# Kernel tuning notes

Measured on AMD Instinct MI355X. Metric: run time of the kernel, lower is better.

Reference implementation:

```python
import jax, jax.numpy as jnp
import numpy as np

N, D = 200000, 256          # num nodes, feature dim
B, NEG = 1024, 64           # batch size, neg_sample_size
S1, S2 = 25, 10             # num_samples for layer 0 and layer 1
OUT = 128                   # per-layer output_dim (concat -> 2*OUT emitted)


def setup_inputs() -> dict:
    key = jax.random.key(0)
    ks = jax.random.split(key, 14)
    inp = {
        "features": jax.random.normal(ks[0], (N, D), jnp.float32),
        "W_self0": jax.random.normal(ks[1], (D, OUT), jnp.float32) / np.sqrt(D).astype(np.float32),
        "W_neigh0": jax.random.normal(ks[2], (D, OUT), jnp.float32) / np.sqrt(D).astype(np.float32),
        "W_self1": jax.random.normal(ks[3], (2 * OUT, OUT), jnp.float32) / np.sqrt(2 * OUT).astype(np.float32),
        "W_neigh1": jax.random.normal(ks[4], (2 * OUT, OUT), jnp.float32) / np.sqrt(2 * OUT).astype(np.float32),
        "s1_0": jax.random.randint(ks[5], (B,), 0, N),
        "s1_1": jax.random.randint(ks[6], (B * S2,), 0, N),
        "s1_2": jax.random.randint(ks[7], (B * S2 * S1,), 0, N),
        "s2_0": jax.random.randint(ks[8], (B,), 0, N),
        "s2_1": jax.random.randint(ks[9], (B * S2,), 0, N),
        "s2_2": jax.random.randint(ks[10], (B * S2 * S1,), 0, N),
        "n_0": jax.random.randint(ks[11], (NEG,), 0, N),
        "n_1": jax.random.randint(ks[12], (NEG * S2,), 0, N),
        "n_2": jax.random.randint(ks[13], (NEG * S2 * S1,), 0, N),
    }
    return inp


def _agg(h_self, h_neigh, Ws, Wn, act):
    """GraphSAGE mean aggregator with concat=True: [M, 2*OUT]."""
    return act(jnp.concatenate([h_self @ Ws, jnp.mean(h_neigh, axis=1) @ Wn], axis=-1))


def _l2norm(x):
    return x / jnp.maximum(jnp.linalg.norm(x, axis=1, keepdims=True), 1e-12)


def reference(features, W_self0, W_neigh0, W_self1, W_neigh1,
              s1_0, s1_1, s1_2, s2_0, s2_1, s2_2, n_0, n_1, n_2):
    def encode(i0, i1, i2, bs):
        h0 = features[i0]                     # [bs, D]
        h1 = features[i1]                     # [bs*S2, D]
        h2 = features[i2]                     # [bs*S2*S1, D]
        # layer 0 (ReLU), applied at hop 0 and hop 1
        g0 = _agg(h0, h1.reshape(bs, S2, D), W_self0, W_neigh0, jax.nn.relu)          # [bs, 2*OUT]
        g1 = _agg(h1, h2.reshape(bs * S2, S1, D), W_self0, W_neigh0, jax.nn.relu)     # [bs*S2, 2*OUT]
        # layer 1 (identity act), hop 0 only
        out = _agg(g0, g1.reshape(bs, S2, 2 * OUT), W_self1, W_neigh1, lambda x: x)   # [bs, 2*OUT]
        return _l2norm(out)

    u1 = encode(s1_0, s1_1, s1_2, B)
    u2 = encode(s2_0, s2_1, s2_2, B)
    un = encode(n_0, n_1, n_2, NEG)

    aff = jnp.sum(u1 * u2, axis=-1)          # [B] positive affinities
    neg_aff = u1 @ un.T                      # [B, NEG]
    # sigmoid cross-entropy: pos label 1, neg label 0
    loss = (jnp.sum(jax.nn.softplus(-aff)) + jnp.sum(jax.nn.softplus(neg_aff))) / B
    return loss, aff, neg_aff, u1
```

## Files before the change

kernel.cpp:

```cpp
#include <hip/hip_runtime.h>
#include <math.h>

#define DD   256
#define BB   1024
#define NEGN 64
#define S1N  25
#define S2N  10
#define OUTN 128
#define NB   (2 * BB + NEGN)
#define NREF1 (2 * BB * S2N + NEGN * S2N)
#define NREF  (NREF1 + NB)
#define NREFP 23280

typedef unsigned int  uint;
typedef unsigned short ushort;
typedef short bf16x8 __attribute__((ext_vector_type(8)));
typedef float f32x4  __attribute__((ext_vector_type(4)));

__device__ __forceinline__ ushort f2bf(float x) {
    uint u = __float_as_uint(x);
    u += 0x7FFFu + ((u >> 16) & 1u);
    return (ushort)(u >> 16);
}
__device__ __forceinline__ float bflo(uint v) { return __uint_as_float(v << 16); }
__device__ __forceinline__ float bfhi(uint v) { return __uint_as_float(v & 0xFFFF0000u); }

__global__ __launch_bounds__(256)
void prep_w_k(const float* __restrict__ Ws0, const float* __restrict__ Wn0,
              ushort* __restrict__ Wt) {
    int col = blockIdx.x;
    int k   = threadIdx.x;
    const float* W = (col < OUTN) ? Ws0 : Wn0;
    int j = col & (OUTN - 1);
    Wt[(size_t)col * 256 + k] = f2bf(W[(size_t)k * OUTN + j]);
}

__global__ __launch_bounds__(256)
void transform_yn_k(const float* __restrict__ feat, const ushort* __restrict__ Wt,
                    ushort* __restrict__ yn) {
    __shared__ ushort As[32 * 256];
    int w = threadIdx.x >> 6, l = threadIdx.x & 63;
    int lane16 = l & 15, kb = (l >> 4) * 8;
    int rh = w >> 1, ch = w & 1;

    bf16x8 bfr[4][8];
#pragma unroll
    for (int c = 0; c < 4; ++c) {
        int col = 128 + ch * 64 + c * 16 + lane16;
#pragma unroll
        for (int kk = 0; kk < 8; ++kk)
            bfr[c][kk] = *(const bf16x8*)(Wt + (size_t)col * 256 + kk * 32 + kb);
    }

    int rr = threadIdx.x >> 4;
    int cq = threadIdx.x & 15;

    for (int tile = 0; tile < 5; ++tile) {
        size_t row0 = (size_t)blockIdx.x * 160 + tile * 32;
        uint2 wr[2][4];
#pragma unroll
        for (int hf = 0; hf < 2; ++hf) {
            int r = hf * 16 + rr;
#pragma unroll
            for (int q = 0; q < 4; ++q) {
                float4 x = *(const float4*)(feat + (row0 + r) * 256 + cq * 16 + q * 4);
                wr[hf][q].x = (uint)f2bf(x.x) | ((uint)f2bf(x.y) << 16);
                wr[hf][q].y = (uint)f2bf(x.z) | ((uint)f2bf(x.w) << 16);
            }
        }
        __syncthreads();
#pragma unroll
        for (int hf = 0; hf < 2; ++hf) {
            int r = hf * 16 + rr;
#pragma unroll
            for (int q = 0; q < 4; ++q) {
                int col = cq * 16 + q * 4;
                *(uint2*)&As[r * 256 + (col ^ ((r & 7) << 3))] = wr[hf][q];
            }
        }
        __syncthreads();

        f32x4 acc[4];
#pragma unroll
        for (int c = 0; c < 4; ++c)
#pragma unroll
            for (int j = 0; j < 4; ++j) acc[c][j] = 0.f;

        int arow = rh * 16 + lane16;
#pragma unroll
        for (int kk = 0; kk < 8; ++kk) {
            int k0 = kk * 32 + kb;
            bf16x8 af = *(const bf16x8*)&As[arow * 256 + (k0 ^ ((arow & 7) << 3))];
#pragma unroll
            for (int c = 0; c < 4; ++c)
                acc[c] = __builtin_amdgcn_mfma_f32_16x16x32_bf16(af, bfr[c][kk], acc[c], 0, 0, 0);
        }

#pragma unroll
        for (int c = 0; c < 4; ++c) {
            int col = ch * 64 + c * 16 + lane16;
#pragma unroll
            for (int j = 0; j < 4; ++j) {
                size_t grow = row0 + rh * 16 + (l >> 4) * 4 + j;
                yn[grow * 128 + col] = f2bf(acc[c][j]);
            }
        }
    }
}

struct SegI {
    const int* i0[3];
    const int* i1[3];
    const int* i2[3];
};

__device__ __forceinline__ int map_ref(int r, const SegI& ix) {
    r = min(r, NREF - 1);
    if (r < 10240) return ix.i1[0][r];
    if (r < 20480) return ix.i1[1][r - 10240];
    if (r < 21120) return ix.i1[2][r - 20480];
    if (r < 22144) return ix.i0[0][r - 21120];
    if (r < 23168) return ix.i0[1][r - 22144];
    return ix.i0[2][r - 23168];
}

__global__ __launch_bounds__(256)
void ysg_k(const float* __restrict__ feat, const ushort* __restrict__ Wt,
           SegI ix, ushort* __restrict__ ysr) {
    __shared__ ushort As[16 * 256];
    int w = threadIdx.x >> 6, l = threadIdx.x & 63;
    int lane16 = l & 15, kb = (l >> 4) * 8;

    bf16x8 bfr[2][8];
#pragma unroll
    for (int c = 0; c < 2; ++c) {
        int col = w * 32 + c * 16 + lane16;
#pragma unroll
        for (int kk = 0; kk < 8; ++kk)
            bfr[c][kk] = *(const bf16x8*)(Wt + (size_t)col * 256 + kk * 32 + kb);
    }

    int rr = threadIdx.x >> 4;
    int cq = threadIdx.x & 15;

    for (int tile = 0; tile < 5; ++tile) {
        int row0 = blockIdx.x * 80 + tile * 16;
        int src = map_ref(row0 + rr, ix);
        uint2 wr[4];
#pragma unroll
        for (int q = 0; q < 4; ++q) {
            float4 x = *(const float4*)(feat + (size_t)src * 256 + cq * 16 + q * 4);
            wr[q].x = (uint)f2bf(x.x) | ((uint)f2bf(x.y) << 16);
            wr[q].y = (uint)f2bf(x.z) | ((uint)f2bf(x.w) << 16);
        }
        __syncthreads();
#pragma unroll
        for (int q = 0; q < 4; ++q) {
            int col = cq * 16 + q * 4;
            *(uint2*)&As[rr * 256 + (col ^ ((rr & 7) << 3))] = wr[q];
        }
        __syncthreads();

        f32x4 acc[2];
#pragma unroll
        for (int c = 0; c < 2; ++c)
#pragma unroll
            for (int j = 0; j < 4; ++j) acc[c][j] = 0.f;

#pragma unroll
        for (int kk = 0; kk < 8; ++kk) {
            int k0 = kk * 32 + kb;
            bf16x8 af = *(const bf16x8*)&As[lane16 * 256 + (k0 ^ ((lane16 & 7) << 3))];
#pragma unroll
            for (int c = 0; c < 2; ++c)
                acc[c] = __builtin_amdgcn_mfma_f32_16x16x32_bf16(af, bfr[c][kk], acc[c], 0, 0, 0);
        }

#pragma unroll
        for (int c = 0; c < 2; ++c) {
            int col = w * 32 + c * 16 + lane16;
#pragma unroll
            for (int j = 0; j < 4; ++j) {
                size_t grow = (size_t)row0 + (l >> 4) * 4 + j;
                ysr[grow * 128 + col] = f2bf(acc[c][j]);
            }
        }
    }
}

__global__ __launch_bounds__(320)
void gather_all_k(const uint* __restrict__ ysrp, const uint* __restrict__ ynp,
                  SegI ix, float* __restrict__ mg1, float* __restrict__ g0) {
    __shared__ float msL[5][64][2];
    __shared__ float mnL[5][64][2];
    __shared__ float gnL[5][64][2];
    int wv = threadIdx.x >> 6;
    int c  = threadIdx.x & 63;
    int b = blockIdx.x;

    int seg, lb;
    if (b < BB) { seg = 0; lb = b; }
    else if (b < 2 * BB) { seg = 1; lb = b - BB; }
    else { seg = 2; lb = b - 2 * BB; }
    const int sbase1[3] = {0, 10240, 20480};
    const int sbase0[3] = {21120, 22144, 23168};
    const int* p1 = ix.i1[seg];
    const int* p2 = ix.i2[seg];

    int i2v = (c < 50) ? p2[(size_t)lb * 250 + wv * 50 + c] : 0;
    int ia = p1[lb * S2N + 2 * wv];
    int ib = p1[lb * S2N + 2 * wv + 1];

    size_t refa = (size_t)(sbase1[seg] + lb * S2N + 2 * wv);
    uint sva = ysrp[refa * 64 + c];
    uint svb = ysrp[(refa + 1) * 64 + c];
    float ms0 = fmaxf(bflo(sva), 0.f) + fmaxf(bflo(svb), 0.f);
    float ms1 = fmaxf(bfhi(sva), 0.f) + fmaxf(bfhi(svb), 0.f);

    uint nva = ynp[(size_t)ia * 64 + c];
    uint nvb = ynp[(size_t)ib * 64 + c];
    float gn0 = bflo(nva) + bflo(nvb);
    float gn1 = bfhi(nva) + bfhi(nvb);

    float mn0, mn1;
    {
        float a0 = 0.f, a1 = 0.f;
#pragma unroll
        for (int t = 0; t < S1N; ++t) {
            int ni = __builtin_amdgcn_readlane(i2v, t);
            uint v = ynp[(size_t)ni * 64 + c];
            a0 += bflo(v); a1 += bfhi(v);
        }
        mn0 = fmaxf(a0 * (1.0f / S1N), 0.f);
        mn1 = fmaxf(a1 * (1.0f / S1N), 0.f);
        a0 = 0.f; a1 = 0.f;
#pragma unroll
        for (int t = S1N; t < 2 * S1N; ++t) {
            int ni = __builtin_amdgcn_readlane(i2v, t);
            uint v = ynp[(size_t)ni * 64 + c];
            a0 += bflo(v); a1 += bfhi(v);
        }
        mn0 += fmaxf(a0 * (1.0f / S1N), 0.f);
        mn1 += fmaxf(a1 * (1.0f / S1N), 0.f);
    }

    msL[wv][c][0] = ms0; msL[wv][c][1] = ms1;
    mnL[wv][c][0] = mn0; mnL[wv][c][1] = mn1;
    gnL[wv][c][0] = gn0; gnL[wv][c][1] = gn1;
    __syncthreads();

    int g = threadIdx.x >> 6;
    const float invS2 = 1.0f / S2N;
    if (g == 0) {
        float s0 = 0.f, s1 = 0.f;
#pragma unroll
        for (int w2 = 0; w2 < 5; ++w2) { s0 += msL[w2][c][0]; s1 += msL[w2][c][1]; }
        float2 o; o.x = s0 * invS2; o.y = s1 * invS2;
        *(float2*)(mg1 + (size_t)b * DD + 2 * c) = o;
    } else if (g == 1) {
        float s0 = 0.f, s1 = 0.f;
#pragma unroll
        for (int w2 = 0; w2 < 5; ++w2) { s0 += mnL[w2][c][0]; s1 += mnL[w2][c][1]; }
        float2 o; o.x = s0 * invS2; o.y = s1 * invS2;
        *(float2*)(mg1 + (size_t)b * DD + 128 + 2 * c) = o;
    } else if (g == 2) {
        float s0 = 0.f, s1 = 0.f;
#pragma unroll
        for (int w2 = 0; w2 < 5; ++w2) { s0 += gnL[w2][c][0]; s1 += gnL[w2][c][1]; }
        float2 o; o.x = fmaxf(s0 * invS2, 0.f); o.y = fmaxf(s1 * invS2, 0.f);
        *(float2*)(g0 + (size_t)b * DD + 128 + 2 * c) = o;
    } else if (g == 3) {
        uint v = ysrp[(size_t)(sbase0[seg] + lb) * 64 + c];
        float2 o; o.x = fmaxf(bflo(v), 0.f); o.y = fmaxf(bfhi(v), 0.f);
        *(float2*)(g0 + (size_t)b * DD + 2 * c) = o;
    }
}

__global__ __launch_bounds__(256)
void final_fused_k(const float* __restrict__ g0, const float* __restrict__ mg1,
                   const float* __restrict__ Ws, const float* __restrict__ Wn,
                   float* __restrict__ u1, float* __restrict__ u2,
                   float* __restrict__ un) {
    constexpr int R = 8;
    __shared__ float xsS[R][DD];
    __shared__ float xnS[R][DD];
    __shared__ float nrmS[R];
    int r0 = blockIdx.x * R;
    int wv = threadIdx.x >> 6;
    int c  = threadIdx.x & 63;

#pragma unroll
    for (int rr = 0; rr < R / 4; ++rr) {
        int r = wv * (R / 4) + rr;
        int row = r0 + r;
        *(float4*)&xsS[r][c * 4] = *(const float4*)(g0 + (size_t)row * DD + c * 4);
        *(float4*)&xnS[r][c * 4] = *(const float4*)(mg1 + (size_t)row * DD + c * 4);
    }
    __syncthreads();

    int j = threadIdx.x & (OUTN - 1);
    const float* Wj = ((threadIdx.x < OUTN) ? Ws : Wn) + j;
    const float (*X)[DD] = (threadIdx.x < OUTN) ? xsS : xnS;
    float acc[R];
#pragma unroll
    for (int r = 0; r < R; ++r) acc[r] = 0.f;
#pragma unroll 4
    for (int k4 = 0; k4 < DD; k4 += 4) {
        float w0 = Wj[(k4 + 0) * OUTN];
        float w1 = Wj[(k4 + 1) * OUTN];
        float w2 = Wj[(k4 + 2) * OUTN];
        float w3 = Wj[(k4 + 3) * OUTN];
#pragma unroll
        for (int r = 0; r < R; ++r) {
            float4 x = *(const float4*)&X[r][k4];
            acc[r] = fmaf(x.x, w0, acc[r]);
            acc[r] = fmaf(x.y, w1, acc[r]);
            acc[r] = fmaf(x.z, w2, acc[r]);
            acc[r] = fmaf(x.w, w3, acc[r]);
        }
    }
    __syncthreads();
    float* sq = &xsS[0][0];
#pragma unroll
    for (int r = 0; r < R; ++r) sq[r * DD + threadIdx.x] = acc[r] * acc[r];
    __syncthreads();
    {
        int g = threadIdx.x >> 5, l = threadIdx.x & 31;
        float s = 0.f;
#pragma unroll
        for (int i = 0; i < 8; ++i) s += sq[g * DD + l + 32 * i];
        s += __shfl_down(s, 16, 64);
        s += __shfl_down(s, 8, 64);
        s += __shfl_down(s, 4, 64);
        s += __shfl_down(s, 2, 64);
        s += __shfl_down(s, 1, 64);
        if (l == 0) nrmS[g] = fmaxf(sqrtf(s), 1e-12f);
    }
    __syncthreads();
#pragma unroll
    for (int r = 0; r < R; ++r) {
        int row = r0 + r;
        float* dst;
        if (row < BB) dst = u1 + (size_t)row * DD;
        else if (row < 2 * BB) dst = u2 + (size_t)(row - BB) * DD;
        else dst = un + (size_t)(row - 2 * BB) * DD;
        dst[threadIdx.x] = acc[r] / nrmS[r];
    }
}

__device__ __forceinline__ float softplus_f(float x) {
    return fmaxf(x, 0.f) + log1pf(expf(-fabsf(x)));
}

__global__ __launch_bounds__(256)
void aff_neg_k(const float* __restrict__ u1, const float* __restrict__ u2,
               const float* __restrict__ un, float* __restrict__ aff,
               float* __restrict__ neg, float* __restrict__ part) {
    __shared__ float u1s[DD];
    __shared__ float red[256];
    int b = blockIdx.x, t = threadIdx.x;
    float av = u1[(size_t)b * DD + t];
    u1s[t] = av;
    red[t] = av * u2[(size_t)b * DD + t];
    __syncthreads();
    for (int s = 128; s > 0; s >>= 1) { if (t < s) red[t] += red[t + s]; __syncthreads(); }
    float affv = red[0];
    __syncthreads();
    if (t == 0) aff[b] = affv;

    int j = t >> 2, q = t & 3;
    float acc = 0.f;
    const float* up = un + (size_t)j * DD + q * 64;
    const float* us = u1s + q * 64;
#pragma unroll
    for (int i = 0; i < 16; ++i) {
        float4 x = *(const float4*)(up + 4 * i);
        float4 y = *(const float4*)(us + 4 * i);
        acc = fmaf(x.x, y.x, acc); acc = fmaf(x.y, y.y, acc);
        acc = fmaf(x.z, y.z, acc); acc = fmaf(x.w, y.w, acc);
    }
    acc += __shfl_down(acc, 2, 64);
    acc += __shfl_down(acc, 1, 64);
    float sp = 0.f;
    if (q == 0) {
        neg[(size_t)b * NEGN + j] = acc;
        sp = softplus_f(acc);
    }
    if (t == 0) sp += softplus_f(-affv);
    red[t] = sp;
    __syncthreads();
    for (int s = 128; s > 0; s >>= 1) { if (t < s) red[t] += red[t + s]; __syncthreads(); }
    if (t == 0) part[b] = red[0];
}

__global__ __launch_bounds__(256)
void loss_final_k(const float* __restrict__ part, float* __restrict__ loss) {
    __shared__ float red[256];
    int t = threadIdx.x;
    red[t] = part[t] + part[t + 256] + part[t + 512] + part[t + 768];
    __syncthreads();
    for (int s = 128; s > 0; s >>= 1) { if (t < s) red[t] += red[t + s]; __syncthreads(); }
    if (t == 0) loss[0] = red[0] / (float)BB;
}

extern "C" void kernel_launch(void* const* d_in, const int* in_sizes, int n_in,
                              void* d_out, int out_size, void* d_ws, size_t ws_size,
                              hipStream_t stream) {
    const float* feat = (const float*)d_in[0];
    const float* Ws0  = (const float*)d_in[1];
    const float* Wn0  = (const float*)d_in[2];
    const float* Ws1  = (const float*)d_in[3];
    const float* Wn1  = (const float*)d_in[4];
    const int* s1_0 = (const int*)d_in[5];
    const int* s1_1 = (const int*)d_in[6];
    const int* s1_2 = (const int*)d_in[7];
    const int* s2_0 = (const int*)d_in[8];
    const int* s2_1 = (const int*)d_in[9];
    const int* s2_2 = (const int*)d_in[10];
    const int* n_0  = (const int*)d_in[11];
    const int* n_1  = (const int*)d_in[12];
    const int* n_2  = (const int*)d_in[13];

    float* out  = (float*)d_out;
    float* loss = out;
    float* aff  = out + 1;
    float* neg  = out + 1 + BB;
    float* u1   = out + 1 + BB + BB * NEGN;

    char* wsb = (char*)d_ws;
    size_t off = 0;
    ushort* Wt  = (ushort*)(wsb + off); off += (size_t)256 * 256 * 2;
    ushort* yn  = (ushort*)(wsb + off); off += (size_t)200000 * 128 * 2;
    ushort* ysr = (ushort*)(wsb + off); off += (size_t)NREFP * 128 * 2;
    float* mg1  = (float*)(wsb + off); off += (size_t)NB * DD * 4;
    float* g0   = (float*)(wsb + off); off += (size_t)NB * DD * 4;
    float* u2   = (float*)(wsb + off); off += (size_t)BB * DD * 4;
    float* un   = (float*)(wsb + off); off += (size_t)NEGN * DD * 4;
    float* part = (float*)(wsb + off); off += (size_t)BB * 4;

    SegI ix;
    ix.i0[0] = s1_0; ix.i0[1] = s2_0; ix.i0[2] = n_0;
    ix.i1[0] = s1_1; ix.i1[1] = s2_1; ix.i1[2] = n_1;
    ix.i2[0] = s1_2; ix.i2[1] = s2_2; ix.i2[2] = n_2;

    prep_w_k<<<256, 256, 0, stream>>>(Ws0, Wn0, Wt);
    transform_yn_k<<<1250, 256, 0, stream>>>(feat, Wt, yn);
    ysg_k<<<291, 256, 0, stream>>>(feat, Wt, ix, ysr);

    gather_all_k<<<NB, 320, 0, stream>>>((const uint*)ysr, (const uint*)yn, ix, mg1, g0);

    final_fused_k<<<NB / 8, 256, 0, stream>>>(g0, mg1, Ws1, Wn1, u1, u2, un);

    aff_neg_k<<<BB, 256, 0, stream>>>(u1, u2, un, aff, neg, part);
    loss_final_k<<<1, 256, 0, stream>>>(part, loss);
}
```

Baseline: 132.5 us.

## Store neighbor projection table in fp8 and merge transform with self-gather kernel

The precomputed neighbor projection of all 200k nodes is now stored as fp8 (e4m3) instead of bf16. This halves the intermediate's write traffic and the gather's random reads. The gather kernel is restructured so each half-wave handles a different neighbor with 4 fp8 values per lane, combined across halves by shuffles. The two projection kernels are fused into one launch with block-range dispatch. The fp8 rounding adds precision loss that may affect tolerance.

Result: faster. 111.3 us (-16.0%).

```diff
diff --git a/kernel.cpp b/kernel.cpp
--- a/kernel.cpp
+++ b/kernel.cpp
@@ -11,11 +11,14 @@
 #define NREF1 (2 * BB * S2N + NEGN * S2N)
 #define NREF  (NREF1 + NB)
 #define NREFP 23280
+#define TBLK 1250
 
 typedef unsigned int  uint;
 typedef unsigned short ushort;
+typedef unsigned char uchar;
 typedef short bf16x8 __attribute__((ext_vector_type(8)));
 typedef float f32x4  __attribute__((ext_vector_type(4)));
+typedef float f32x2  __attribute__((ext_vector_type(2)));
 
 __device__ __forceinline__ ushort f2bf(float x) {
     uint u = __float_as_uint(x);
@@ -24,6 +27,53 @@
 }
 __device__ __forceinline__ float bflo(uint v) { return __uint_as_float(v << 16); }
 __device__ __forceinline__ float bfhi(uint v) { return __uint_as_float(v & 0xFFFF0000u); }
+
+#if __has_builtin(__builtin_amdgcn_cvt_pk_fp8_f32) && __has_builtin(__builtin_amdgcn_cvt_pk_f32_fp8)
+__device__ __forceinline__ uchar fp8_enc(float x) {
+    return (uchar)(__builtin_amdgcn_cvt_pk_fp8_f32(x, x, 0, false) & 0xff);
+}
+template <bool HI>
+__device__ __forceinline__ f32x2 fp8_dec2(uint v) {
+    return __builtin_amdgcn_cvt_pk_f32_fp8(v, HI);
+}
+#else
+__device__ __forceinline__ uchar fp8_enc(float x) {
+    uint u = __float_as_uint(x);
+    uint s = (u >> 24) & 0x80u;
+    float a = fabsf(x);
+    if (a >= 448.f) return (uchar)(s | 0x7Eu);
+    if (a < 0.0009765625f) return (uchar)s;
+    int e; float fm = frexpf(a, &e);
+    int pe = e - 1;
+    uint code;
+    if (pe >= -6) {
+        int mi = (int)rintf((fm * 2.0f - 1.0f) * 8.0f);
+        if (mi == 8) { mi = 0; pe += 1; }
+        if (pe > 8) return (uchar)(s | 0x7Eu);
+        code = ((uint)(pe + 7) << 3) | (uint)mi;
+        if (code > 0x7Eu) code = 0x7Eu;
+    } else {
+        int mi = (int)rintf(a * 512.0f);
+        code = (mi >= 8) ? 8u : (uint)mi;
+    }
+    return (uchar)(s | code);
+}
+__device__ __forceinline__ float fp8_dec1(uint b) {
+    uint s = (b & 0x80u) << 24;
+    uint em = b & 0x7fu;
+    if (em >= 8) return __uint_as_float(s | ((em + 960u) << 20));
+    float v = (float)em * 0.001953125f;
+    return (b & 0x80u) ? -v : v;
+}
+template <bool HI>
+__device__ __forceinline__ f32x2 fp8_dec2(uint v) {
+    f32x2 r;
+    uint w = HI ? (v >> 16) : v;
+    r.x = fp8_dec1(w & 0xffu);
+    r.y = fp8_dec1((w >> 8) & 0xffu);
+    return r;
+}
+#endif
 
 __global__ __launch_bounds__(256)
 void prep_w_k(const float* __restrict__ Ws0, const float* __restrict__ Wn0,
@@ -35,79 +85,6 @@
     Wt[(size_t)col * 256 + k] = f2bf(W[(size_t)k * OUTN + j]);
 }
 
-__global__ __launch_bounds__(256)
-void transform_yn_k(const float* __restrict__ feat, const ushort* __restrict__ Wt,
-                    ushort* __restrict__ yn) {
-    __shared__ ushort As[32 * 256];
-    int w = threadIdx.x >> 6, l = threadIdx.x & 63;
-    int lane16 = l & 15, kb = (l >> 4) * 8;
-    int rh = w >> 1, ch = w & 1;
-
-    bf16x8 bfr[4][8];
-#pragma unroll
-    for (int c = 0; c < 4; ++c) {
-        int col = 128 + ch * 64 + c * 16 + lane16;
-#pragma unroll
-        for (int kk = 0; kk < 8; ++kk)
-            bfr[c][kk] = *(const bf16x8*)(Wt + (size_t)col * 256 + kk * 32 + kb);
-    }
-
-    int rr = threadIdx.x >> 4;
-    int cq = threadIdx.x & 15;
-
-    for (int tile = 0; tile < 5; ++tile) {
-        size_t row0 = (size_t)blockIdx.x * 160 + tile * 32;
-        uint2 wr[2][4];
-#pragma unroll
-        for (int hf = 0; hf < 2; ++hf) {
-            int r = hf * 16 + rr;
-#pragma unroll
-            for (int q = 0; q < 4; ++q) {
-                float4 x = *(const float4*)(feat + (row0 + r) * 256 + cq * 16 + q * 4);
-                wr[hf][q].x = (uint)f2bf(x.x) | ((uint)f2bf(x.y) << 16);
-                wr[hf][q].y = (uint)f2bf(x.z) | ((uint)f2bf(x.w) << 16);
-            }
-        }
-        __syncthreads();
-#pragma unroll
-        for (int hf = 0; hf < 2; ++hf) {
-            int r = hf * 16 + rr;
-#pragma unroll
-            for (int q = 0; q < 4; ++q) {
-                int col = cq * 16 + q * 4;
-                *(uint2*)&As[r * 256 + (col ^ ((r & 7) << 3))] = wr[hf][q];
-            }
-        }
-        __syncthreads();
-
-        f32x4 acc[4];
-#pragma unroll
-        for (int c = 0; c < 4; ++c)
-#pragma unroll
-            for (int j = 0; j < 4; ++j) acc[c][j] = 0.f;
-
-        int arow = rh * 16 + lane16;
-#pragma unroll
-        for (int kk = 0; kk < 8; ++kk) {
-            int k0 = kk * 32 + kb;
-            bf16x8 af = *(const bf16x8*)&As[arow * 256 + (k0 ^ ((arow & 7) << 3))];
-#pragma unroll
-            for (int c = 0; c < 4; ++c)
-                acc[c] = __builtin_amdgcn_mfma_f32_16x16x32_bf16(af, bfr[c][kk], acc[c], 0, 0, 0);
-        }
-
-#pragma unroll
-        for (int c = 0; c < 4; ++c) {
-            int col = ch * 64 + c * 16 + lane16;
-#pragma unroll
-            for (int j = 0; j < 4; ++j) {
-                size_t grow = row0 + rh * 16 + (l >> 4) * 4 + j;
-                yn[grow * 128 + col] = f2bf(acc[c][j]);
-            }
-        }
-    }
-}
-
 struct SegI {
     const int* i0[3];
     const int* i1[3];
@@ -125,77 +102,143 @@
 }
 
 __global__ __launch_bounds__(256)
-void ysg_k(const float* __restrict__ feat, const ushort* __restrict__ Wt,
-           SegI ix, ushort* __restrict__ ysr) {
-    __shared__ ushort As[16 * 256];
+void trans_ysg_k(const float* __restrict__ feat, const ushort* __restrict__ Wt,
+                 SegI ix, uchar* __restrict__ yn8, ushort* __restrict__ ysr) {
+    __shared__ ushort As[32 * 256];
     int w = threadIdx.x >> 6, l = threadIdx.x & 63;
     int lane16 = l & 15, kb = (l >> 4) * 8;
 
-    bf16x8 bfr[2][8];
-#pragma unroll
-    for (int c = 0; c < 2; ++c) {
-        int col = w * 32 + c * 16 + lane16;
-#pragma unroll
-        for (int kk = 0; kk < 8; ++kk)
-            bfr[c][kk] = *(const bf16x8*)(Wt + (size_t)col * 256 + kk * 32 + kb);
-    }
-
-    int rr = threadIdx.x >> 4;
-    int cq = threadIdx.x & 15;
-
-    for (int tile = 0; tile < 5; ++tile) {
-        int row0 = blockIdx.x * 80 + tile * 16;
-        int src = map_ref(row0 + rr, ix);
-        uint2 wr[4];
-#pragma unroll
-        for (int q = 0; q < 4; ++q) {
-            float4 x = *(const float4*)(feat + (size_t)src * 256 + cq * 16 + q * 4);
-            wr[q].x = (uint)f2bf(x.x) | ((uint)f2bf(x.y) << 16);
-            wr[q].y = (uint)f2bf(x.z) | ((uint)f2bf(x.w) << 16);
-        }
-        __syncthreads();
-#pragma unroll
-        for (int q = 0; q < 4; ++q) {
-            int col = cq * 16 + q * 4;
-            *(uint2*)&As[rr * 256 + (col ^ ((rr & 7) << 3))] = wr[q];
-        }
-        __syncthreads();
-
-        f32x4 acc[2];
-#pragma unroll
-        for (int c = 0; c < 2; ++c)
-#pragma unroll
-            for (int j = 0; j < 4; ++j) acc[c][j] = 0.f;
-
-#pragma unroll
-        for (int kk = 0; kk < 8; ++kk) {
-            int k0 = kk * 32 + kb;
-            bf16x8 af = *(const bf16x8*)&As[lane16 * 256 + (k0 ^ ((lane16 & 7) << 3))];
-#pragma unroll
-            for (int c = 0; c < 2; ++c)
-                acc[c] = __builtin_amdgcn_mfma_f32_16x16x32_bf16(af, bfr[c][kk], acc[c], 0, 0, 0);
-        }
-
+    if (blockIdx.x < TBLK) {
+        int rh = w >> 1, ch = w & 1;
+        bf16x8 bfr[4][8];
+#pragma unroll
+        for (int c = 0; c < 4; ++c) {
+            int col = 128 + ch * 64 + c * 16 + lane16;
+#pragma unroll
+            for (int kk = 0; kk < 8; ++kk)
+                bfr[c][kk] = *(const bf16x8*)(Wt + (size_t)col * 256 + kk * 32 + kb);
+        }
+        int rr = threadIdx.x >> 4;
+        int cq = threadIdx.x & 15;
+
+        for (int tile = 0; tile < 5; ++tile) {
+            size_t row0 = (size_t)blockIdx.x * 160 + tile * 32;
+            uint2 wr[2][4];
+#pragma unroll
+            for (int hf = 0; hf < 2; ++hf) {
+                int r = hf * 16 + rr;
+#pragma unroll
+                for (int q = 0; q < 4; ++q) {
+                    float4 x = *(const float4*)(feat + (row0 + r) * 256 + cq * 16 + q * 4);
+                    wr[hf][q].x = (uint)f2bf(x.x) | ((uint)f2bf(x.y) << 16);
+                    wr[hf][q].y = (uint)f2bf(x.z) | ((uint)f2bf(x.w) << 16);
+                }
+            }
+            __syncthreads();
+#pragma unroll
+            for (int hf = 0; hf < 2; ++hf) {
+                int r = hf * 16 + rr;
+#pragma unroll
+                for (int q = 0; q < 4; ++q) {
+                    int col = cq * 16 + q * 4;
+                    *(uint2*)&As[r * 256 + (col ^ ((r & 7) << 3))] = wr[hf][q];
+                }
+            }
+            __syncthreads();
+
+            f32x4 acc[4];
+#pragma unroll
+            for (int c = 0; c < 4; ++c)
+#pragma unroll
+                for (int j = 0; j < 4; ++j) acc[c][j] = 0.f;
+
+            int arow = rh * 16 + lane16;
+#pragma unroll
+            for (int kk = 0; kk < 8; ++kk) {
+                int k0 = kk * 32 + kb;
+                bf16x8 af = *(const bf16x8*)&As[arow * 256 + (k0 ^ ((arow & 7) << 3))];
+#pragma unroll
+                for (int c = 0; c < 4; ++c)
+                    acc[c] = __builtin_amdgcn_mfma_f32_16x16x32_bf16(af, bfr[c][kk], acc[c], 0, 0, 0);
+            }
+
+#pragma unroll
+            for (int c = 0; c < 4; ++c) {
+                int col = ch * 64 + c * 16 + lane16;
+#pragma unroll
+                for (int j = 0; j < 4; ++j) {
+                    size_t grow = row0 + rh * 16 + (l >> 4) * 4 + j;
+                    yn8[grow * 128 + col] = fp8_enc(acc[c][j]);
+                }
+            }
+        }
+    } else {
+        int bid = blockIdx.x - TBLK;
+        bf16x8 bfr[2][8];
 #pragma unroll
         for (int c = 0; c < 2; ++c) {
             int col = w * 32 + c * 16 + lane16;
 #pragma unroll
-            for (int j = 0; j < 4; ++j) {
-                size_t grow = (size_t)row0 + (l >> 4) * 4 + j;
-                ysr[grow * 128 + col] = f2bf(acc[c][j]);
+            for (int kk = 0; kk < 8; ++kk)
+                bfr[c][kk] = *(const bf16x8*)(Wt + (size_t)col * 256 + kk * 32 + kb);
+        }
+        int rr = threadIdx.x >> 4;
+        int cq = threadIdx.x & 15;
+
+        for (int tile = 0; tile < 5; ++tile) {
+            int row0 = bid * 80 + tile * 16;
+            int src = map_ref(row0 + rr, ix);
+            uint2 wr[4];
+#pragma unroll
+            for (int q = 0; q < 4; ++q) {
+                float4 x = *(const float4*)(feat + (size_t)src * 256 + cq * 16 + q * 4);
+                wr[q].x = (uint)f2bf(x.x) | ((uint)f2bf(x.y) << 16);
+                wr[q].y = (uint)f2bf(x.z) | ((uint)f2bf(x.w) << 16);
+            }
+            __syncthreads();
+#pragma unroll
+            for (int q = 0; q < 4; ++q) {
+                int col = cq * 16 + q * 4;
+                *(uint2*)&As[rr * 256 + (col ^ ((rr & 7) << 3))] = wr[q];
+            }
+            __syncthreads();
+
+            f32x4 acc[2];
+#pragma unroll
+            for (int c = 0; c < 2; ++c)
+#pragma unroll
+                for (int j = 0; j < 4; ++j) acc[c][j] = 0.f;
+
+#pragma unroll
+            for (int kk = 0; kk < 8; ++kk) {
+                int k0 = kk * 32 + kb;
+                bf16x8 af = *(const bf16x8*)&As[lane16 * 256 + (k0 ^ ((lane16 & 7) << 3))];
+#pragma unroll
+                for (int c = 0; c < 2; ++c)
+                    acc[c] = __builtin_amdgcn_mfma_f32_16x16x32_bf16(af, bfr[c][kk], acc[c], 0, 0, 0);
+            }
+
+#pragma unroll
+            for (int c = 0; c < 2; ++c) {
+                int col = w * 32 + c * 16 + lane16;
+#pragma unroll
+                for (int j = 0; j < 4; ++j) {
+                    size_t grow = (size_t)row0 + (l >> 4) * 4 + j;
+                    ysr[grow * 128 + col] = f2bf(acc[c][j]);
+                }
             }
         }
     }
 }
 
 __global__ __launch_bounds__(320)
-void gather_all_k(const uint* __restrict__ ysrp, const uint* __restrict__ ynp,
+void gather_all_k(const uint* __restrict__ ysrp, const uint* __restrict__ yn8u,
                   SegI ix, float* __restrict__ mg1, float* __restrict__ g0) {
     __shared__ float msL[5][64][2];
-    __shared__ float mnL[5][64][2];
-    __shared__ float gnL[5][64][2];
+    __shared__ float mnL[5][32][4];
+    __shared__ float gnL[5][32][4];
     int wv = threadIdx.x >> 6;
-    int c  = threadIdx.x & 63;
+    int l  = threadIdx.x & 63;
     int b = blockIdx.x;
 
     int seg, lb;
@@ -207,49 +250,62 @@
     const int* p1 = ix.i1[seg];
     const int* p2 = ix.i2[seg];
 
-    int i2v = (c < 50) ? p2[(size_t)lb * 250 + wv * 50 + c] : 0;
+    int i2v = (l < 50) ? p2[(size_t)lb * 250 + wv * 50 + l] : 0;
     int ia = p1[lb * S2N + 2 * wv];
     int ib = p1[lb * S2N + 2 * wv + 1];
 
+    int half = l >> 5;
+    int cg   = l & 31;
+
+    float accA[4] = {0.f, 0.f, 0.f, 0.f};
+    float accB[4] = {0.f, 0.f, 0.f, 0.f};
+#pragma unroll
+    for (int p = 0; p < 25; ++p) {
+        int rlo = __builtin_amdgcn_readlane(i2v, 2 * p);
+        int rhi = __builtin_amdgcn_readlane(i2v, 2 * p + 1);
+        int ni = half ? rhi : rlo;
+        uint v = yn8u[(size_t)ni * 32 + cg];
+        f32x2 f01 = fp8_dec2<false>(v);
+        f32x2 f23 = fp8_dec2<true>(v);
+        if (p < 12) {
+            accA[0] += f01.x; accA[1] += f01.y; accA[2] += f23.x; accA[3] += f23.y;
+        } else if (p > 12) {
+            accB[0] += f01.x; accB[1] += f01.y; accB[2] += f23.x; accB[3] += f23.y;
+        } else {
+            if (!half) { accA[0] += f01.x; accA[1] += f01.y; accA[2] += f23.x; accA[3] += f23.y; }
+            else       { accB[0] += f01.x; accB[1] += f01.y; accB[2] += f23.x; accB[3] += f23.y; }
+        }
+    }
+    float mnv[4], gnv[4];
+    {
+        int ng = half ? ib : ia;
+        uint v = yn8u[(size_t)ng * 32 + cg];
+        f32x2 f01 = fp8_dec2<false>(v);
+        f32x2 f23 = fp8_dec2<true>(v);
+        gnv[0] = f01.x; gnv[1] = f01.y; gnv[2] = f23.x; gnv[3] = f23.y;
+    }
+#pragma unroll
+    for (int k = 0; k < 4; ++k) {
+        accA[k] += __shfl_xor(accA[k], 32, 64);
+        accB[k] += __shfl_xor(accB[k], 32, 64);
+        gnv[k]  += __shfl_xor(gnv[k], 32, 64);
+        mnv[k] = fmaxf(accA[k] * (1.0f / S1N), 0.f) + fmaxf(accB[k] * (1.0f / S1N), 0.f);
+    }
+
     size_t refa = (size_t)(sbase1[seg] + lb * S2N + 2 * wv);
-    uint sva = ysrp[refa * 64 + c];
-    uint svb = ysrp[(refa + 1) * 64 + c];
+    uint sva = ysrp[refa * 64 + l];
+    uint svb = ysrp[(refa + 1) * 64 + l];
     float ms0 = fmaxf(bflo(sva), 0.f) + fmaxf(bflo(svb), 0.f);
     float ms1 = fmaxf(bfhi(sva), 0.f) + fmaxf(bfhi(svb), 0.f);
 
-    uint nva = ynp[(size_t)ia * 64 + c];
-    uint nvb = ynp[(size_t)ib * 64 + c];
-    float gn0 = bflo(nva) + bflo(nvb);
-    float gn1 = bfhi(nva) + bfhi(nvb);
-
-    float mn0, mn1;
-    {
-        float a0 = 0.f, a1 = 0.f;
-#pragma unroll
-        for (int t = 0; t < S1N; ++t) {
-            int ni = __builtin_amdgcn_readlane(i2v, t);
-            uint v = ynp[(size_t)ni * 64 + c];
-            a0 += bflo(v); a1 += bfhi(v);
-        }
-        mn0 = fmaxf(a0 * (1.0f / S1N), 0.f);
-        mn1 = fmaxf(a1 * (1.0f / S1N), 0.f);
-        a0 = 0.f; a1 = 0.f;
-#pragma unroll
-        for (int t = S1N; t < 2 * S1N; ++t) {
-            int ni = __builtin_amdgcn_readlane(i2v, t);
-            uint v = ynp[(size_t)ni * 64 + c];
-            a0 += bflo(v); a1 += bfhi(v);
-        }
-        mn0 += fmaxf(a0 * (1.0f / S1N), 0.f);
-        mn1 += fmaxf(a1 * (1.0f / S1N), 0.f);
-    }
-
-    msL[wv][c][0] = ms0; msL[wv][c][1] = ms1;
-    mnL[wv][c][0] = mn0; mnL[wv][c][1] = mn1;
-    gnL[wv][c][0] = gn0; gnL[wv][c][1] = gn1;
-    __syncthreads();
-
-    int g = threadIdx.x >> 6;
+    msL[wv][l][0] = ms0; msL[wv][l][1] = ms1;
+    if (l < 32) {
+#pragma unroll
+        for (int k = 0; k < 4; ++k) { mnL[wv][l][k] = mnv[k]; gnL[wv][l][k] = gnv[k]; }
+    }
+    __syncthreads();
+
+    int g = threadIdx.x >> 6, c = l;
     const float invS2 = 1.0f / S2N;
     if (g == 0) {
         float s0 = 0.f, s1 = 0.f;
@@ -258,17 +314,28 @@
         float2 o; o.x = s0 * invS2; o.y = s1 * invS2;
         *(float2*)(mg1 + (size_t)b * DD + 2 * c) = o;
     } else if (g == 1) {
-        float s0 = 0.f, s1 = 0.f;
-#pragma unroll
-        for (int w2 = 0; w2 < 5; ++w2) { s0 += mnL[w2][c][0]; s1 += mnL[w2][c][1]; }
-        float2 o; o.x = s0 * invS2; o.y = s1 * invS2;
-        *(float2*)(mg1 + (size_t)b * DD + 128 + 2 * c) = o;
+        if (c < 32) {
+            float4 o;
+            float s[4] = {0.f, 0.f, 0.f, 0.f};
+#pragma unroll
+            for (int w2 = 0; w2 < 5; ++w2)
+#pragma unroll
+                for (int k = 0; k < 4; ++k) s[k] += mnL[w2][c][k];
+            o.x = s[0] * invS2; o.y = s[1] * invS2; o.z = s[2] * invS2; o.w = s[3] * invS2;
+            *(float4*)(mg1 + (size_t)b * DD + 128 + 4 * c) = o;
+        }
     } else if (g == 2) {
-        float s0 = 0.f, s1 = 0.f;
-#pragma unroll
-        for (int w2 = 0; w2 < 5; ++w2) { s0 += gnL[w2][c][0]; s1 += gnL[w2][c][1]; }
-        float2 o; o.x = fmaxf(s0 * invS2, 0.f); o.y = fmaxf(s1 * invS2, 0.f);
-        *(float2*)(g0 + (size_t)b * DD + 128 + 2 * c) = o;
+        if (c < 32) {
+            float4 o;
+            float s[4] = {0.f, 0.f, 0.f, 0.f};
+#pragma unroll
+            for (int w2 = 0; w2 < 5; ++w2)
+#pragma unroll
+                for (int k = 0; k < 4; ++k) s[k] += gnL[w2][c][k];
+            o.x = fmaxf(s[0] * invS2, 0.f); o.y = fmaxf(s[1] * invS2, 0.f);
+            o.z = fmaxf(s[2] * invS2, 0.f); o.w = fmaxf(s[3] * invS2, 0.f);
+            *(float4*)(g0 + (size_t)b * DD + 128 + 4 * c) = o;
+        }
     } else if (g == 3) {
         uint v = ysrp[(size_t)(sbase0[seg] + lb) * 64 + c];
         float2 o; o.x = fmaxf(bflo(v), 0.f); o.y = fmaxf(bfhi(v), 0.f);
@@ -325,16 +392,16 @@
     for (int r = 0; r < R; ++r) sq[r * DD + threadIdx.x] = acc[r] * acc[r];
     __syncthreads();
     {
-        int g = threadIdx.x >> 5, l = threadIdx.x & 31;
+        int g = threadIdx.x >> 5, ll = threadIdx.x & 31;
         float s = 0.f;
 #pragma unroll
-        for (int i = 0; i < 8; ++i) s += sq[g * DD + l + 32 * i];
+        for (int i = 0; i < 8; ++i) s += sq[g * DD + ll + 32 * i];
         s += __shfl_down(s, 16, 64);
         s += __shfl_down(s, 8, 64);
         s += __shfl_down(s, 4, 64);
         s += __shfl_down(s, 2, 64);
         s += __shfl_down(s, 1, 64);
-        if (l == 0) nrmS[g] = fmaxf(sqrtf(s), 1e-12f);
+        if (ll == 0) nrmS[g] = fmaxf(sqrtf(s), 1e-12f);
     }
     __syncthreads();
 #pragma unroll
@@ -430,7 +497,7 @@
     char* wsb = (char*)d_ws;
     size_t off = 0;
     ushort* Wt  = (ushort*)(wsb + off); off += (size_t)256 * 256 * 2;
-    ushort* yn  = (ushort*)(wsb + off); off += (size_t)200000 * 128 * 2;
+    uchar*  yn8 = (uchar*)(wsb + off);  off += (size_t)200000 * 128;
     ushort* ysr = (ushort*)(wsb + off); off += (size_t)NREFP * 128 * 2;
     float* mg1  = (float*)(wsb + off); off += (size_t)NB * DD * 4;
     float* g0   = (float*)(wsb + off); off += (size_t)NB * DD * 4;
@@ -444,10 +511,9 @@
     ix.i2[0] = s1_2; ix.i2[1] = s2_2; ix.i2[2] = n_2;
 
     prep_w_k<<<256, 256, 0, stream>>>(Ws0, Wn0, Wt);
-    transform_yn_k<<<1250, 256, 0, stream>>>(feat, Wt, yn);
-    ysg_k<<<291, 256, 0, stream>>>(feat, Wt, ix, ysr);
-
-    gather_all_k<<<NB, 320, 0, stream>>>((const uint*)ysr, (const uint*)yn, ix, mg1, g0);
+    trans_ysg_k<<<TBLK + 291, 256, 0, stream>>>(feat, Wt, ix, yn8, ysr);
+
+    gather_all_k<<<NB, 320, 0, stream>>>((const uint*)ysr, (const uint*)yn8, ix, mg1, g0);
 
     final_fused_k<<<NB / 8, 256, 0, stream>>>(g0, mg1, Ws1, Wn1, u1, u2, un);
 
```
